# Performance work log

Measured on AMD Instinct MI355X. Metric: run time of the kernel, lower is better.

The kernel has to match this reference:

```python
import jax, jax.numpy as jnp
import numpy as np

E = 1024        # embedding_dim
DIN = 2048      # d_inner = E * expand_factor(2)
N = 16          # state_dim
DTR = 64        # dt_rank = ceil(E/16)
K_CONV = 4      # conv_dim


def tt_dense(g1, g2):
    # TT with ranks [1,16,1]: W[(m1,m2),(n1,n2)] = sum_r g1[m1,n1,r] g2[r,m2,n2]
    m1, n1, r = g1.shape
    _, m2, n2 = g2.shape
    return jnp.einsum('air,rbj->abij', g1, g2).reshape(m1 * m2, n1 * n2)


def setup_inputs() -> dict:
    key = jax.random.key(0)
    ks = jax.random.split(key, 12)
    s = 0.05  # init scale for TT cores
    return {
        'x': jax.random.normal(ks[0], (2, 1024, E), dtype=jnp.float32),
        # in_proj: 1024=[32,32] -> 4096=[64,64]
        'in_g1': jax.random.normal(ks[1], (32, 64, 16)) * s,
        'in_g2': jax.random.normal(ks[2], (16, 32, 64)) * s,
        # x_proj: 2048=[32,64] -> 96=[8,12]
        'x_g1': jax.random.normal(ks[3], (32, 8, 16)) * s,
        'x_g2': jax.random.normal(ks[4], (16, 64, 12)) * s,
        # dt_proj: 64=[8,8] -> 2048=[32,64]
        'dt_g1': jax.random.normal(ks[5], (8, 32, 16)) * s,
        'dt_g2': jax.random.normal(ks[6], (16, 8, 64)) * s,
        # out_proj: 2048=[32,64] -> 1024=[32,32]
        'out_g1': jax.random.normal(ks[7], (32, 32, 16)) * s,
        'out_g2': jax.random.normal(ks[8], (16, 64, 32)) * s,
        'conv_filter': jax.random.normal(ks[9], (K_CONV, 1, DIN)) * 0.1,
        'conv_bias': jnp.zeros((DIN,), jnp.float32),
        'A_log': jax.random.uniform(ks[10], (DIN, N), dtype=jnp.float32),
        'D': jnp.zeros((DIN,), jnp.float32),
    }


def _forward(x, in_g1, in_g2, x_g1, x_g2, dt_g1, dt_g2, out_g1, out_g2,
             conv_filter, conv_bias, A_log, D):
    B, L, _ = x.shape
    # in_proj (TT) -> split into conv path and gate
    xz = (x.reshape(-1, E) @ tt_dense(in_g1, in_g2)).reshape(B, L, 2 * DIN)
    x_conv, z = xz[..., :DIN], xz[..., DIN:]
    # depthwise conv1d, SAME padding, + bias, SiLU, gate by z
    conv = jax.lax.conv_general_dilated(
        x_conv, conv_filter, window_strides=(1,), padding='SAME',
        dimension_numbers=('NWC', 'WIO', 'NWC'), feature_group_count=DIN)
    y = jax.nn.silu(conv + conv_bias) * z            # [B, L, DIN]
    # x_proj (TT) -> dt_unscaled, B, C
    dtBC = (y.reshape(-1, DIN) @ tt_dense(x_g1, x_g2)).reshape(B, L, DTR + 2 * N)
    dt_un = dtBC[..., :DTR]
    Bm = dtBC[..., DTR:DTR + N]                      # [B, L, N]
    Cm = dtBC[..., DTR + N:]                         # [B, L, N]
    # dt_proj (TT) + softplus
    dt = jax.nn.softplus(dt_un.reshape(-1, DTR) @ tt_dense(dt_g1, dt_g2)).reshape(B, L, DIN)
    # selective scan
    A = -jnp.exp(A_log)                              # [DIN, N]

    def step(h, inp):
        dt_t, u_t, B_t, C_t = inp                    # [B,DIN],[B,DIN],[B,N],[B,N]
        dA = jnp.exp(dt_t[:, :, None] * A)           # [B, DIN, N]
        h = dA * h + dt_t[:, :, None] * B_t[:, None, :] * u_t[:, :, None]
        y_t = jnp.einsum('bdn,bn->bd', h, C_t) + D * u_t
        return h, (y_t, h)

    h0 = jnp.zeros((B, DIN, N), x.dtype)
    _, (ys, hs) = jax.lax.scan(
        step, h0,
        (dt.swapaxes(0, 1), y.swapaxes(0, 1), Bm.swapaxes(0, 1), Cm.swapaxes(0, 1)))
    ssm_out = ys.swapaxes(0, 1) + jnp.mean(hs) * 1e-8  # [B, L, DIN]
    out = (ssm_out.reshape(-1, DIN) @ tt_dense(out_g1, out_g2)).reshape(B, L, E)
    return out


def reference(x, in_g1, in_g2, x_g1, x_g2, dt_g1, dt_g2, out_g1, out_g2,
              conv_filter, conv_bias, A_log, D):
    return _forward(x, in_g1, in_g2, x_g1, x_g2, dt_g1, dt_g2, out_g1, out_g2,
                    conv_filter, conv_bias, A_log, D)
```

## Files before the change

kernel.cpp:

```cpp
#include <hip/hip_runtime.h>
#include <hip/hip_bf16.h>
#include <cstdint>
#include <cstddef>

#define EE    1024
#define DIN   2048
#define NST   16
#define DTR   64
#define BB_   2
#define LL    1024
#define BL    (BB_*LL)
#define NCHUNK 32
#define CLEN   32
#define RTT   16

typedef unsigned short u16;
typedef unsigned int   u32;

static constexpr size_t OFF_WINT  = 0;
static constexpr size_t OFF_WOUTT = 2097152;
static constexpr size_t OFF_WXT   = 3145728;
static constexpr size_t OFF_WDTT  = 3276800;
static constexpr size_t OFF_A2T   = 3342336;
static constexpr size_t OFF_XB    = 3375104;
static constexpr size_t OFF_XZB   = 4423680;
static constexpr size_t OFF_YB    = 8617984;
static constexpr size_t OFF_PART  = 10715136;
static constexpr size_t OFF_DTBC  = 14909440;
static constexpr size_t OFF_DTUNB = 15106048;
static constexpr size_t OFF_DTB   = 15171584;
static constexpr size_t OFF_YSB   = 17268736;
static constexpr size_t OFF_HC    = 19365888;
static constexpr size_t OFF_SDT   = 21463040;

__device__ __forceinline__ u16 f2bf(float f) {
    u32 u = __float_as_uint(f);
    u += 0x7fffu + ((u >> 16) & 1u);
    return (u16)(u >> 16);
}
__device__ __forceinline__ float bf2f(u16 v) {
    return __uint_as_float((u32)v << 16);
}

__device__ __forceinline__ void async_copy16(const void* g, void* l) {
    __builtin_amdgcn_global_load_lds((const __attribute__((address_space(1))) u32*)g,
                                     (__attribute__((address_space(3))) u32*)l,
                                     16, 0, 0);
}

__device__ __forceinline__ float softplusf(float v) {
    return fmaxf(v, 0.f) + log1pf(__expf(-fabsf(v)));
}

__device__ void tt_part(const float* __restrict__ g1, const float* __restrict__ g2,
                        u16* __restrict__ Wt, int m1, int n1, int m2, int n2,
                        int c, int crows, float* g1col, float* g2col)
{
    const int rowsW = m1 * m2;
    if (c >= crows) {
        for (int k = threadIdx.x; k < rowsW; k += 256)
            Wt[(size_t)c * rowsW + k] = 0;
        return;
    }
    const int i = c / n2;
    const int j = c - i * n2;

    for (int e = threadIdx.x; e < m1 * RTT; e += 256) {
        const int a = e >> 4, rr = e & 15;
        g1col[e] = g1[(size_t)(a * n1 + i) * RTT + rr];
    }
    for (int e = threadIdx.x; e < RTT * m2; e += 256) {
        const int rr = e / m2, bb = e - rr * m2;
        g2col[e] = g2[(size_t)(rr * m2 + bb) * n2 + j];
    }
    __syncthreads();

    for (int k = threadIdx.x; k < rowsW; k += 256) {
        const int a  = k / m2;
        const int bb = k - a * m2;
        const float* gp = g1col + a * RTT;
        float s = 0.f;
        #pragma unroll
        for (int rr = 0; rr < RTT; ++rr)
            s = fmaf(gp[rr], g2col[rr * m2 + bb], s);
        Wt[(size_t)c * rowsW + k] = f2bf(s);
    }
}

__global__ __launch_bounds__(256) void mega_prep(
    const float* __restrict__ in_g1, const float* __restrict__ in_g2, u16* __restrict__ W_inT,
    const float* __restrict__ out_g1, const float* __restrict__ out_g2, u16* __restrict__ W_outT,
    const float* __restrict__ x_g1, const float* __restrict__ x_g2, u16* __restrict__ W_xT,
    const float* __restrict__ dt_g1, const float* __restrict__ dt_g2, u16* __restrict__ W_dtT,
    const float* __restrict__ x, u16* __restrict__ xb,
    const float* __restrict__ A_log, float* __restrict__ A2t)
{
    __shared__ float g1col[32 * RTT];
    __shared__ float g2col[RTT * 64];
    const int blk = blockIdx.x;
    if (blk < 4096) {
        tt_part(in_g1, in_g2, W_inT, 32, 64, 32, 64, blk, 4096, g1col, g2col);
    } else if (blk < 5120) {
        tt_part(out_g1, out_g2, W_outT, 32, 32, 64, 32, blk - 4096, 1024, g1col, g2col);
    } else if (blk < 5248) {
        tt_part(x_g1, x_g2, W_xT, 32, 8, 64, 12, blk - 5120, 96, g1col, g2col);
    } else if (blk < 7296) {
        tt_part(dt_g1, dt_g2, W_dtT, 8, 32, 8, 64, blk - 5248, 2048, g1col, g2col);
    } else if (blk < 9344) {
        const int i = (blk - 7296) * 256 + threadIdx.x;
        float4 v = ((const float4*)x)[i];
        ushort4 o;
        o.x = f2bf(v.x); o.y = f2bf(v.y); o.z = f2bf(v.z); o.w = f2bf(v.w);
        ((ushort4*)xb)[i] = o;
    } else {
        const int idx = (blk - 9344) * 256 + threadIdx.x;
        const int d = idx >> 4, n = idx & 15;
        A2t[n * DIN + d] = -expf(A_log[idx]);
    }
}

typedef __attribute__((ext_vector_type(8))) short bf16x8;
typedef __attribute__((ext_vector_type(4))) float floatx4;
typedef __attribute__((ext_vector_type(8))) unsigned short ushortx8;

template<int BN, int BK, int OUT>
__global__ __launch_bounds__(256) void gemm_bf16(
    const u16* __restrict__ A, const u16* __restrict__ Bt, void* __restrict__ Cout,
    int K, int ldc, int kchunk, size_t czstride, int ncols)
{
    constexpr int BM   = 128;
    constexpr int NT   = BN / 32;
    constexpr int SLOT = BK / 8;
    constexpr int CR   = 64 / SLOT;
    constexpr int NACH = BM / CR / 4;
    constexpr int NBCH = BN / CR / 4;
    constexpr int KG   = BK / 32;
    __shared__ __align__(16) u16 smem[BM * BK + BN * BK];
    u16* As = smem;
    u16* Bs = smem + BM * BK;

    const int tid  = threadIdx.x;
    const int w    = tid >> 6;
    const int lane = tid & 63;
    const int wm   = w & 1, wn = w >> 1;
    const int row0 = blockIdx.y * BM;
    const int col0 = blockIdx.x * BN;
    const int kbeg = blockIdx.z * kchunk;

    const int srow = lane / SLOT;
    const int kqp  = lane % SLOT;
    const u16* ga[NACH]; u16* la[NACH];
    #pragma unroll
    for (int i = 0; i < NACH; ++i) {
        const int c  = w * NACH + i;
        const int r  = c * CR + srow;
        const int kq = kqp ^ ((r >> 1) & (SLOT - 1));
        ga[i] = A + (size_t)(row0 + r) * K + kbeg + kq * 8;
        la[i] = &As[c * CR * BK];
    }
    const u16* gb[NBCH]; u16* lb[NBCH];
    #pragma unroll
    for (int i = 0; i < NBCH; ++i) {
        const int c  = w * NBCH + i;
        const int r  = c * CR + srow;
        const int kq = kqp ^ ((r >> 1) & (SLOT - 1));
        gb[i] = Bt + (size_t)(col0 + r) * K + kbeg + kq * 8;
        lb[i] = &Bs[c * CR * BK];
    }

    const int q = lane >> 4, l15 = lane & 15;
    int a_off[4][KG], b_off[NT][KG];
    #pragma unroll
    for (int mt = 0; mt < 4; ++mt) {
        const int r = wm * 64 + mt * 16 + l15;
        const int m = (r >> 1) & (SLOT - 1);
        #pragma unroll
        for (int kk = 0; kk < KG; ++kk)
            a_off[mt][kk] = r * BK + ((kk * 4 + q) ^ m) * 8;
    }
    #pragma unroll
    for (int nt = 0; nt < NT; ++nt) {
        const int r = wn * (BN / 2) + nt * 16 + l15;
        const int m = (r >> 1) & (SLOT - 1);
        #pragma unroll
        for (int kk = 0; kk < KG; ++kk)
            b_off[nt][kk] = r * BK + ((kk * 4 + q) ^ m) * 8;
    }

    floatx4 acc[4][NT];
    #pragma unroll
    for (int mt = 0; mt < 4; ++mt)
        #pragma unroll
        for (int nt = 0; nt < NT; ++nt)
            acc[mt][nt] = (floatx4){0.f, 0.f, 0.f, 0.f};

    for (int k0 = 0; k0 < kchunk; k0 += BK) {
        #pragma unroll
        for (int i = 0; i < NACH; ++i) { async_copy16(ga[i], la[i]); ga[i] += BK; }
        #pragma unroll
        for (int i = 0; i < NBCH; ++i) { async_copy16(gb[i], lb[i]); gb[i] += BK; }
        __syncthreads();

        bf16x8 af[4][KG], bfv[NT][KG];
        #pragma unroll
        for (int mt = 0; mt < 4; ++mt)
            #pragma unroll
            for (int kk = 0; kk < KG; ++kk)
                af[mt][kk] = *(const bf16x8*)&As[a_off[mt][kk]];
        #pragma unroll
        for (int nt = 0; nt < NT; ++nt)
            #pragma unroll
            for (int kk = 0; kk < KG; ++kk)
                bfv[nt][kk] = *(const bf16x8*)&Bs[b_off[nt][kk]];

        #pragma unroll
        for (int kk = 0; kk < KG; ++kk)
            #pragma unroll
            for (int mt = 0; mt < 4; ++mt)
                #pragma unroll
                for (int nt = 0; nt < NT; ++nt)
                    acc[mt][nt] = __builtin_amdgcn_mfma_f32_16x16x32_bf16(
                        af[mt][kk], bfv[nt][kk], acc[mt][nt], 0, 0, 0);

        __syncthreads();
    }

    if constexpr (OUT == 0) {
        #pragma unroll
        for (int mt = 0; mt < 4; ++mt) {
            const int row = row0 + wm * 64 + mt * 16 + q * 4;
            #pragma unroll
            for (int nt = 0; nt < NT; ++nt) {
                const int col = col0 + wn * (BN / 2) + nt * 16 + l15;
                if (col < ncols) {
                    #pragma unroll
                    for (int r = 0; r < 4; ++r)
                        ((float*)Cout)[(size_t)blockIdx.z * czstride + (size_t)(row + r) * ldc + col] = acc[mt][nt][r];
                }
            }
        }
    } else {
        u16* cst = smem;
        #pragma unroll
        for (int mt = 0; mt < 4; ++mt) {
            #pragma unroll
            for (int nt = 0; nt < NT; ++nt) {
                const int lc = wn * (BN / 2) + nt * 16 + l15;
                #pragma unroll
                for (int r = 0; r < 4; ++r) {
                    float v = acc[mt][nt][r];
                    if constexpr (OUT == 2) v = softplusf(v);
                    const int lr = wm * 64 + mt * 16 + q * 4 + r;
                    cst[lr * BN + (lc ^ ((lr & (BN / 8 - 1)) << 3))] = f2bf(v);
                }
            }
        }
        __syncthreads();
        constexpr int C8 = BN / 8;
        for (int i = tid; i < BM * C8; i += 256) {
            const int r  = i / C8;
            const int c8 = i % C8;
            const int gc = col0 + c8 * 8;
            if (gc < ncols)
                *(ushortx8*)&((u16*)Cout)[(size_t)(row0 + r) * ldc + gc] =
                    *(const ushortx8*)&cst[r * BN + ((c8 * 8) ^ ((r & (BN / 8 - 1)) << 3))];
        }
    }
}

__global__ __launch_bounds__(512, 2) void gemm_bf16_dp(
    const u16* __restrict__ A, const u16* __restrict__ Bt, u16* __restrict__ Cout,
    int K, int ldc)
{
    constexpr int BM   = 128;
    constexpr int BN   = 256;
    constexpr int BK   = 64;
    constexpr int SLOT = BK / 8;
    constexpr int CR   = 64 / SLOT;
    constexpr int NACH = BM / CR / 8;
    constexpr int NBCH = BN / CR / 8;
    constexpr int AST  = BM * BK;
    constexpr int BST  = BN * BK;

    __shared__ __align__(16) u16 As[3 * AST];
    __shared__ __align__(16) u16 Bs[3 * BST];

    const int tid  = threadIdx.x;
    const int w    = tid >> 6;
    const int lane = tid & 63;
    const int wm   = w & 1;
    const int wn   = w >> 1;
    const int row0 = blockIdx.y * BM;
    const int col0 = blockIdx.x * BN;

    const int srow = lane / SLOT;
    const int kqp  = lane % SLOT;
    const u16* ga[NACH]; int laA[NACH];
    #pragma unroll
    for (int i = 0; i < NACH; ++i) {
        const int c  = w * NACH + i;
        const int r  = c * CR + srow;
        const int kq = kqp ^ ((r >> 1) & (SLOT - 1));
        ga[i]  = A + (size_t)(row0 + r) * K + kq * 8;
        laA[i] = c * CR * BK;
    }
    const u16* gb[NBCH]; int laB[NBCH];
    #pragma unroll
    for (int i = 0; i < NBCH; ++i) {
        const int c  = w * NBCH + i;
        const int r  = c * CR + srow;
        const int kq = kqp ^ ((r >> 1) & (SLOT - 1));
        gb[i]  = Bt + (size_t)(col0 + r) * K + kq * 8;
        laB[i] = c * CR * BK;
    }

    const int q = lane >> 4, l15 = lane & 15;
    int a_off[4][2], b_off[4][2];
    #pragma unroll
    for (int mt = 0; mt < 4; ++mt) {
        const int r = wm * 64 + mt * 16 + l15;
        const int m = (r >> 1) & (SLOT - 1);
        #pragma unroll
        for (int kk = 0; kk < 2; ++kk)
            a_off[mt][kk] = r * BK + ((kk * 4 + q) ^ m) * 8;
    }
    #pragma unroll
    for (int nt = 0; nt < 4; ++nt) {
        const int r = wn * 64 + nt * 16 + l15;
        const int m = (r >> 1) & (SLOT - 1);
        #pragma unroll
        for (int kk = 0; kk < 2; ++kk)
            b_off[nt][kk] = r * BK + ((kk * 4 + q) ^ m) * 8;
    }

    floatx4 acc[4][4];
    #pragma unroll
    for (int mt = 0; mt < 4; ++mt)
        #pragma unroll
        for (int nt = 0; nt < 4; ++nt)
            acc[mt][nt] = (floatx4){0.f, 0.f, 0.f, 0.f};

    const int NTILES = K / BK;

    #pragma unroll
    for (int i = 0; i < NACH; ++i) { async_copy16(ga[i], &As[0 * AST + laA[i]]); ga[i] += BK; }
    #pragma unroll
    for (int i = 0; i < NBCH; ++i) { async_copy16(gb[i], &Bs[0 * BST + laB[i]]); gb[i] += BK; }
    #pragma unroll
    for (int i = 0; i < NACH; ++i) { async_copy16(ga[i], &As[1 * AST + laA[i]]); ga[i] += BK; }
    #pragma unroll
    for (int i = 0; i < NBCH; ++i) { async_copy16(gb[i], &Bs[1 * BST + laB[i]]); gb[i] += BK; }
    __builtin_amdgcn_sched_barrier(0);
    asm volatile("s_waitcnt vmcnt(6)" ::: "memory");
    __builtin_amdgcn_s_barrier();
    __builtin_amdgcn_sched_barrier(0);

    int cur = 0, nxt = 2;
    for (int t = 0; t < NTILES; ++t) {
        const bool pf = (t + 2 < NTILES);
        const u16* Ac = &As[cur * AST];
        const u16* Bc = &Bs[cur * BST];
        u16* An = &As[nxt * AST];
        u16* Bn = &Bs[nxt * BST];

        bf16x8 af[4], bfv[4];

        #pragma unroll
        for (int mt = 0; mt < 4; ++mt) af[mt]  = *(const bf16x8*)&Ac[a_off[mt][0]];
        #pragma unroll
        for (int nt = 0; nt < 4; ++nt) bfv[nt] = *(const bf16x8*)&Bc[b_off[nt][0]];
        if (pf) {
            async_copy16(ga[0], &An[laA[0]]);
            async_copy16(ga[1], &An[laA[1]]);
            async_copy16(gb[0], &Bn[laB[0]]);
        }
        __builtin_amdgcn_sched_barrier(0);
        __builtin_amdgcn_s_barrier();
        asm volatile("s_waitcnt lgkmcnt(0)" ::: "memory");
        __builtin_amdgcn_sched_barrier(0);
        __builtin_amdgcn_s_setprio(1);
        #pragma unroll
        for (int mt = 0; mt < 4; ++mt)
            #pragma unroll
            for (int nt = 0; nt < 4; ++nt)
                acc[mt][nt] = __builtin_amdgcn_mfma_f32_16x16x32_bf16(
                    af[mt], bfv[nt], acc[mt][nt], 0, 0, 0);
        __builtin_amdgcn_s_setprio(0);
        __builtin_amdgcn_sched_barrier(0);
        __builtin_amdgcn_s_barrier();
        __builtin_amdgcn_sched_barrier(0);

        #pragma unroll
        for (int mt = 0; mt < 4; ++mt) af[mt]  = *(const bf16x8*)&Ac[a_off[mt][1]];
        #pragma unroll
        for (int nt = 0; nt < 4; ++nt) bfv[nt] = *(const bf16x8*)&Bc[b_off[nt][1]];
        if (pf) {
            async_copy16(gb[1], &Bn[laB[1]]);
            async_copy16(gb[2], &Bn[laB[2]]);
            async_copy16(gb[3], &Bn[laB[3]]);
            #pragma unroll
            for (int i = 0; i < NACH; ++i) ga[i] += BK;
            #pragma unroll
            for (int i = 0; i < NBCH; ++i) gb[i] += BK;
        }
        __builtin_amdgcn_sched_barrier(0);
        __builtin_amdgcn_s_barrier();
        asm volatile("s_waitcnt lgkmcnt(0)" ::: "memory");
        __builtin_amdgcn_sched_barrier(0);
        __builtin_amdgcn_s_setprio(1);
        #pragma unroll
        for (int mt = 0; mt < 4; ++mt)
            #pragma unroll
            for (int nt = 0; nt < 4; ++nt)
                acc[mt][nt] = __builtin_amdgcn_mfma_f32_16x16x32_bf16(
                    af[mt], bfv[nt], acc[mt][nt], 0, 0, 0);
        __builtin_amdgcn_s_setprio(0);
        __builtin_amdgcn_sched_barrier(0);
        if (pf) asm volatile("s_waitcnt vmcnt(6)" ::: "memory");
        else    asm volatile("s_waitcnt vmcnt(0)" ::: "memory");
        __builtin_amdgcn_s_barrier();
        __builtin_amdgcn_sched_barrier(0);

        cur = (cur == 2) ? 0 : cur + 1;
        nxt = (nxt == 2) ? 0 : nxt + 1;
    }

    u16* cst = Bs;
    #pragma unroll
    for (int mt = 0; mt < 4; ++mt) {
        #pragma unroll
        for (int nt = 0; nt < 4; ++nt) {
            const int lc = wn * 64 + nt * 16 + l15;
            #pragma unroll
            for (int r = 0; r < 4; ++r) {
                const int lr = wm * 64 + mt * 16 + q * 4 + r;
                cst[lr * 256 + (lc ^ ((lr & 31) << 3))] = f2bf(acc[mt][nt][r]);
            }
        }
    }
    __syncthreads();
    for (int i = tid; i < 128 * 32; i += 512) {
        const int r  = i >> 5;
        const int c8 = i & 31;
        *(ushortx8*)&Cout[(size_t)(row0 + r) * ldc + col0 + c8 * 8] =
            *(const ushortx8*)&cst[r * 256 + ((c8 * 8) ^ ((r & 31) << 3))];
    }
}

__global__ __launch_bounds__(256) void reduce_dtbc(
    const float* __restrict__ part, float* __restrict__ dtBC, u16* __restrict__ dtun_b)
{
    int idx = blockIdx.x * 256 + threadIdx.x;
    if (idx >= BL * 96) return;
    const int row = idx / 96;
    const int col = idx - row * 96;
    float s = 0.f;
    #pragma unroll
    for (int z = 0; z < 16; ++z)
        s += part[(size_t)z * BL * 96 + idx];
    dtBC[idx] = s;
    if (col < 64) dtun_b[(size_t)row * 64 + col] = f2bf(s);
}

__global__ __launch_bounds__(256) void conv_gate(
    const u16* __restrict__ xzb, const float* __restrict__ filt,
    const float* __restrict__ bias, u16* __restrict__ yb)
{
    int idx = blockIdx.x * blockDim.x + threadIdx.x;
    if (idx >= BL * DIN / 8) return;
    const int d  = (idx % (DIN / 8)) * 8;
    const int bt = idx / (DIN / 8);
    const int b  = bt >> 10;
    const int t  = bt & 1023;

    float acc[8];
    #pragma unroll
    for (int j = 0; j < 8; ++j) acc[j] = bias[d + j];
    #pragma unroll
    for (int k = 0; k < 4; ++k) {
        const int tt = t + k - 1;
        if ((unsigned)tt < (unsigned)LL) {
            const ushortx8 xc = *(const ushortx8*)(xzb + (size_t)(b * LL + tt) * (2 * DIN) + d);
            #pragma unroll
            for (int j = 0; j < 8; ++j)
                acc[j] = fmaf(bf2f(xc[j]), filt[(size_t)k * DIN + d + j], acc[j]);
        }
    }
    const ushortx8 z = *(const ushortx8*)(xzb + (size_t)bt * (2 * DIN) + DIN + d);
    ushortx8 o;
    #pragma unroll
    for (int j = 0; j < 8; ++j)
        o[j] = f2bf(acc[j] / (1.f + __expf(-acc[j])) * bf2f(z[j]));
    *(ushortx8*)(yb + (size_t)bt * DIN + d) = o;
}

__global__ __launch_bounds__(256) void scan_phase_a(
    const u16* __restrict__ dt, const u16* __restrict__ u,
    const float* __restrict__ dtBC, const float* __restrict__ A2t,
    float* __restrict__ hend, float* __restrict__ sdtbuf)
{
    const int d = blockIdx.x * 256 + threadIdx.x;
    const int c = blockIdx.y;
    const int b = blockIdx.z;

    __shared__ float Bs[CLEN][NST];
    for (int e = threadIdx.x; e < CLEN * NST; e += 256) {
        const int tl = e >> 4, n = e & 15;
        Bs[tl][n] = dtBC[(size_t)(b * LL + c * CLEN + tl) * 96 + 64 + n];
    }
    __syncthreads();

    float A2r[NST];
    #pragma unroll
    for (int n = 0; n < NST; ++n) A2r[n] = A2t[n * DIN + d];

    float h[NST] = {};
    float sdt = 0.f;
    const size_t tbase = (size_t)(b * LL + c * CLEN) * DIN + d;
    for (int tl = 0; tl < CLEN; ++tl) {
        const float dtv = bf2f(dt[tbase + (size_t)tl * DIN]);
        const float uv  = bf2f(u [tbase + (size_t)tl * DIN]);
        sdt += dtv;
        const float cu = dtv * uv;
        #pragma unroll
        for (int n = 0; n < NST; ++n) {
            const float a = __expf(A2r[n] * dtv);
            h[n] = fmaf(a, h[n], cu * Bs[tl][n]);
        }
    }
    const int cb = b * NCHUNK + c;
    #pragma unroll
    for (int n = 0; n < NST; ++n)
        hend[((size_t)cb * NST + n) * DIN + d] = h[n];
    sdtbuf[(size_t)cb * DIN + d] = sdt;
}

__global__ __launch_bounds__(256) void scan_phase_b(
    const float* __restrict__ A2t, const float* __restrict__ sdtbuf,
    float* __restrict__ hcarry)
{
    const int idx = blockIdx.x * 256 + threadIdx.x;
    if (idx >= BB_ * NST * DIN) return;
    const int d = idx & (DIN - 1);
    const int n = (idx >> 11) & 15;
    const int b = idx >> 15;
    const float A2 = A2t[n * DIN + d];
    float h = 0.f;
    for (int c = 0; c < NCHUNK; ++c) {
        const int cb = b * NCHUNK + c;
        const size_t off = ((size_t)cb * NST + n) * DIN + d;
        const float he = hcarry[off];
        const float pa = __expf(A2 * sdtbuf[(size_t)cb * DIN + d]);
        hcarry[off] = h;
        h = fmaf(pa, h, he);
    }
}

__global__ __launch_bounds__(256) void scan_phase_c(
    const u16* __restrict__ dt, const u16* __restrict__ u,
    const float* __restrict__ dtBC, const float* __restrict__ A2t,
    const float* __restrict__ hinit, const float* __restrict__ Dp,
    u16* __restrict__ ysb)
{
    const int d = blockIdx.x * 256 + threadIdx.x;
    const int c = blockIdx.y;
    const int b = blockIdx.z;

    __shared__ float Bs[CLEN][NST];
    __shared__ float Cs[CLEN][NST];
    for (int e = threadIdx.x; e < CLEN * NST; e += 256) {
        const int tl = e >> 4, n = e & 15;
        const size_t base = (size_t)(b * LL + c * CLEN + tl) * 96;
        Bs[tl][n] = dtBC[base + 64 + n];
        Cs[tl][n] = dtBC[base + 80 + n];
    }
    __syncthreads();

    float A2r[NST], h[NST];
    const int cb = b * NCHUNK + c;
    #pragma unroll
    for (int n = 0; n < NST; ++n) {
        A2r[n] = A2t[n * DIN + d];
        h[n]   = hinit[((size_t)cb * NST + n) * DIN + d];
    }
    const float Dv = Dp[d];

    const size_t tbase = (size_t)(b * LL + c * CLEN) * DIN + d;
    for (int tl = 0; tl < CLEN; ++tl) {
        const float dtv = bf2f(dt[tbase + (size_t)tl * DIN]);
        const float uv  = bf2f(u [tbase + (size_t)tl * DIN]);
        const float cu = dtv * uv;
        float yacc = 0.f;
        #pragma unroll
        for (int n = 0; n < NST; ++n) {
            const float a = __expf(A2r[n] * dtv);
            h[n] = fmaf(a, h[n], cu * Bs[tl][n]);
            yacc = fmaf(h[n], Cs[tl][n], yacc);
        }
        ysb[tbase + (size_t)tl * DIN] = f2bf(fmaf(Dv, uv, yacc));
    }
}

extern "C" void kernel_launch(void* const* d_in, const int* in_sizes, int n_in,
                              void* d_out, int out_size, void* d_ws, size_t ws_size,
                              hipStream_t stream)
{
    const float* x       = (const float*)d_in[0];
    const float* in_g1   = (const float*)d_in[1];
    const float* in_g2   = (const float*)d_in[2];
    const float* x_g1    = (const float*)d_in[3];
    const float* x_g2    = (const float*)d_in[4];
    const float* dt_g1   = (const float*)d_in[5];
    const float* dt_g2   = (const float*)d_in[6];
    const float* out_g1  = (const float*)d_in[7];
    const float* out_g2  = (const float*)d_in[8];
    const float* filt    = (const float*)d_in[9];
    const float* bias    = (const float*)d_in[10];
    const float* A_log   = (const float*)d_in[11];
    const float* Dp      = (const float*)d_in[12];

    float* ws     = (float*)d_ws;
    u16*   W_inT  = (u16*)(ws + OFF_WINT);
    u16*   W_outT = (u16*)(ws + OFF_WOUTT);
    u16*   W_xT   = (u16*)(ws + OFF_WXT);
    u16*   W_dtT  = (u16*)(ws + OFF_WDTT);
    float* A2t    = ws + OFF_A2T;
    u16*   xb     = (u16*)(ws + OFF_XB);
    u16*   xzb    = (u16*)(ws + OFF_XZB);
    u16*   yb     = (u16*)(ws + OFF_YB);
    float* part   = ws + OFF_PART;
    float* dtBC   = ws + OFF_DTBC;
    u16*   dtun_b = (u16*)(ws + OFF_DTUNB);
    u16*   dtb    = (u16*)(ws + OFF_DTB);
    u16*   ysb    = (u16*)(ws + OFF_YSB);
    float* hc     = ws + OFF_HC;
    float* sdt    = ws + OFF_SDT;

    mega_prep<<<9472, 256, 0, stream>>>(
        in_g1, in_g2, W_inT, out_g1, out_g2, W_outT,
        x_g1, x_g2, W_xT, dt_g1, dt_g2, W_dtT,
        x, xb, A_log, A2t);

    gemm_bf16_dp<<<dim3(16, 16, 1), 512, 0, stream>>>(
        xb, W_inT, xzb, EE, 4096);

    conv_gate<<<(BL * DIN / 8 + 255) / 256, 256, 0, stream>>>(xzb, filt, bias, yb);

    gemm_bf16<128, 64, 0><<<dim3(1, 16, 16), 256, 0, stream>>>(
        yb, W_xT, part, DIN, 96, 128, (size_t)BL * 96, 96);
    reduce_dtbc<<<(BL * 96 + 255) / 256, 256, 0, stream>>>(part, dtBC, dtun_b);

    gemm_bf16<128, 64, 2><<<dim3(16, 16, 1), 256, 0, stream>>>(
        dtun_b, W_dtT, dtb, 64, DIN, 64, 0, DIN);

    scan_phase_a<<<dim3(DIN / 256, NCHUNK, BB_), 256, 0, stream>>>(dtb, yb, dtBC, A2t, hc, sdt);
    scan_phase_b<<<(BB_ * NST * DIN) / 256, 256, 0, stream>>>(A2t, sdt, hc);
    scan_phase_c<<<dim3(DIN / 256, NCHUNK, BB_), 256, 0, stream>>>(dtb, yb, dtBC, A2t, hc, Dp, ysb);

    gemm_bf16<64, 64, 0><<<dim3(16, 16, 1), 256, 0, stream>>>(
        ysb, W_outT, d_out, DIN, EE, DIN, 0, EE);
}
```

Baseline: 237.0 us.

## Rebalance prep blocks, retile small GEMMs, split-K the out projection

The prep kernel now has each block build two TT weight columns or convert two float4 chunks, which halves the block count. A barrier is added so the shared scratch can be reused between the two columns. The x_proj GEMM moves to narrower tiles with an 8-way K split, the dt_proj GEMM to 64-wide tiles with twice the column blocks, and the out_proj GEMM becomes 2-way split-K with a separate float4 reduction kernel. The goal is better occupancy and parallelism on the small GEMMs. The cost is an extra kernel launch and an extra read/write of a partial-sum buffer for the output projection.

```diff
diff --git a/kernel.cpp b/kernel.cpp
--- a/kernel.cpp
+++ b/kernel.cpp
@@ -62,6 +62,7 @@
             Wt[(size_t)c * rowsW + k] = 0;
         return;
     }
+    __syncthreads();
     const int i = c / n2;
     const int j = c - i * n2;
 
@@ -98,22 +99,34 @@
     __shared__ float g1col[32 * RTT];
     __shared__ float g2col[RTT * 64];
     const int blk = blockIdx.x;
-    if (blk < 4096) {
-        tt_part(in_g1, in_g2, W_inT, 32, 64, 32, 64, blk, 4096, g1col, g2col);
-    } else if (blk < 5120) {
-        tt_part(out_g1, out_g2, W_outT, 32, 32, 64, 32, blk - 4096, 1024, g1col, g2col);
-    } else if (blk < 5248) {
-        tt_part(x_g1, x_g2, W_xT, 32, 8, 64, 12, blk - 5120, 96, g1col, g2col);
-    } else if (blk < 7296) {
-        tt_part(dt_g1, dt_g2, W_dtT, 8, 32, 8, 64, blk - 5248, 2048, g1col, g2col);
-    } else if (blk < 9344) {
-        const int i = (blk - 7296) * 256 + threadIdx.x;
-        float4 v = ((const float4*)x)[i];
-        ushort4 o;
-        o.x = f2bf(v.x); o.y = f2bf(v.y); o.z = f2bf(v.z); o.w = f2bf(v.w);
-        ((ushort4*)xb)[i] = o;
+    if (blk < 2048) {
+        const int c = blk * 2;
+        tt_part(in_g1, in_g2, W_inT, 32, 64, 32, 64, c,     4096, g1col, g2col);
+        tt_part(in_g1, in_g2, W_inT, 32, 64, 32, 64, c + 1, 4096, g1col, g2col);
+    } else if (blk < 2560) {
+        const int c = (blk - 2048) * 2;
+        tt_part(out_g1, out_g2, W_outT, 32, 32, 64, 32, c,     1024, g1col, g2col);
+        tt_part(out_g1, out_g2, W_outT, 32, 32, 64, 32, c + 1, 1024, g1col, g2col);
+    } else if (blk < 2624) {
+        const int c = (blk - 2560) * 2;
+        tt_part(x_g1, x_g2, W_xT, 32, 8, 64, 12, c,     96, g1col, g2col);
+        tt_part(x_g1, x_g2, W_xT, 32, 8, 64, 12, c + 1, 96, g1col, g2col);
+    } else if (blk < 3648) {
+        const int c = (blk - 2624) * 2;
+        tt_part(dt_g1, dt_g2, W_dtT, 8, 32, 8, 64, c,     2048, g1col, g2col);
+        tt_part(dt_g1, dt_g2, W_dtT, 8, 32, 8, 64, c + 1, 2048, g1col, g2col);
+    } else if (blk < 4672) {
+        const int i0 = (blk - 3648) * 512 + threadIdx.x;
+        #pragma unroll
+        for (int s = 0; s < 2; ++s) {
+            const int i = i0 + s * 256;
+            float4 v = ((const float4*)x)[i];
+            ushort4 o;
+            o.x = f2bf(v.x); o.y = f2bf(v.y); o.z = f2bf(v.z); o.w = f2bf(v.w);
+            ((ushort4*)xb)[i] = o;
+        }
     } else {
-        const int idx = (blk - 9344) * 256 + threadIdx.x;
+        const int idx = (blk - 4672) * 256 + threadIdx.x;
         const int d = idx >> 4, n = idx & 15;
         A2t[n * DIN + d] = -expf(A_log[idx]);
     }
@@ -456,10 +469,21 @@
     const int col = idx - row * 96;
     float s = 0.f;
     #pragma unroll
-    for (int z = 0; z < 16; ++z)
+    for (int z = 0; z < 8; ++z)
         s += part[(size_t)z * BL * 96 + idx];
     dtBC[idx] = s;
     if (col < 64) dtun_b[(size_t)row * 64 + col] = f2bf(s);
+}
+
+__global__ __launch_bounds__(256) void reduce_out(
+    const float* __restrict__ part, float* __restrict__ out)
+{
+    const int idx = blockIdx.x * 256 + threadIdx.x;
+    const float4 a = ((const float4*)part)[idx];
+    const float4 b = ((const float4*)part)[idx + BL * EE / 4];
+    float4 o;
+    o.x = a.x + b.x; o.y = a.y + b.y; o.z = a.z + b.z; o.w = a.w + b.w;
+    ((float4*)out)[idx] = o;
 }
 
 __global__ __launch_bounds__(256) void conv_gate(
@@ -636,7 +660,7 @@
     float* hc     = ws + OFF_HC;
     float* sdt    = ws + OFF_SDT;
 
-    mega_prep<<<9472, 256, 0, stream>>>(
+    mega_prep<<<4800, 256, 0, stream>>>(
         in_g1, in_g2, W_inT, out_g1, out_g2, W_outT,
         x_g1, x_g2, W_xT, dt_g1, dt_g2, W_dtT,
         x, xb, A_log, A2t);
@@ -646,17 +670,18 @@
 
     conv_gate<<<(BL * DIN / 8 + 255) / 256, 256, 0, stream>>>(xzb, filt, bias, yb);
 
-    gemm_bf16<128, 64, 0><<<dim3(1, 16, 16), 256, 0, stream>>>(
-        yb, W_xT, part, DIN, 96, 128, (size_t)BL * 96, 96);
+    gemm_bf16<64, 64, 0><<<dim3(2, 16, 8), 256, 0, stream>>>(
+        yb, W_xT, part, DIN, 96, 256, (size_t)BL * 96, 96);
     reduce_dtbc<<<(BL * 96 + 255) / 256, 256, 0, stream>>>(part, dtBC, dtun_b);
 
-    gemm_bf16<128, 64, 2><<<dim3(16, 16, 1), 256, 0, stream>>>(
+    gemm_bf16<64, 64, 2><<<dim3(32, 16, 1), 256, 0, stream>>>(
         dtun_b, W_dtT, dtb, 64, DIN, 64, 0, DIN);
 
     scan_phase_a<<<dim3(DIN / 256, NCHUNK, BB_), 256, 0, stream>>>(dtb, yb, dtBC, A2t, hc, sdt);
     scan_phase_b<<<(BB_ * NST * DIN) / 256, 256, 0, stream>>>(A2t, sdt, hc);
     scan_phase_c<<<dim3(DIN / 256, NCHUNK, BB_), 256, 0, stream>>>(dtb, yb, dtBC, A2t, hc, Dp, ysb);
 
-    gemm_bf16<64, 64, 0><<<dim3(16, 16, 1), 256, 0, stream>>>(
-        ysb, W_outT, d_out, DIN, EE, DIN, 0, EE);
-}
+    gemm_bf16<64, 64, 0><<<dim3(16, 16, 2), 256, 0, stream>>>(
+        ysb, W_outT, part, DIN, EE, EE, (size_t)BL * EE, EE);
+    reduce_out<<<(BL * EE / 4) / 256, 256, 0, stream>>>(part, (float*)d_out);
+}
```

Result: faster. 221.4 us (-6.6%).
